# Performance work log

Measured on AMD Instinct MI355X. Metric: run time of the kernel, lower is better.

The kernel has to match this reference:

```python
import jax, jax.numpy as jnp
import numpy as np

# camera / raster constants
N = 10000            # gaussians
W = 256
H = 256
FX = 200.0
FY = 200.0
TILE = 16
NTX = W // TILE
NTY = H // TILE
NT = NTX * NTY       # 256 tiles
P = TILE * TILE      # 256 pixels per tile
K = 256              # max gaussians kept per tile
NEAR = 0.3
MAGIC = 1.2          # frustum expansion factor from project_culling
LP = 0.3 / (FX * FX) # low-pass filter added to 2D covariance diagonal


def quat_to_rot(q):
    w, x, y, z = q[:, 0], q[:, 1], q[:, 2], q[:, 3]
    r0 = jnp.stack([1 - 2 * (y * y + z * z), 2 * (x * y - w * z), 2 * (x * z + w * y)], -1)
    r1 = jnp.stack([2 * (x * y + w * z), 1 - 2 * (x * x + z * z), 2 * (y * z - w * x)], -1)
    r2 = jnp.stack([2 * (x * z - w * y), 2 * (y * z + w * x), 1 - 2 * (x * x + y * y)], -1)
    return jnp.stack([r0, r1, r2], axis=1)  # [N,3,3]


def splat_forward(pos, rgb, opacity, quaternion, scale, w2c_r, w2c_t):
    # ---- project + frustum cull (global_culling) ----
    q = quaternion / jnp.linalg.norm(quaternion, axis=-1, keepdims=True)
    R = quat_to_rot(q)
    sigma = jnp.exp(scale)                               # normalize_scale
    cov3d = jnp.einsum('nij,nj,nkj->nik', R, sigma * sigma, R)
    p_cam = pos @ w2c_r.T + w2c_t                        # [N,3]
    x, y, z = p_cam[:, 0], p_cam[:, 1], p_cam[:, 2]
    zc = jnp.maximum(z, 1e-6)
    half_w = W * MAGIC / 2 / FX
    half_h = H * MAGIC / 2 / FY
    mean2d = jnp.stack([x / zc, y / zc], -1)             # camera-plane coords
    in_frustum = (z > NEAR) & (jnp.abs(mean2d[:, 0]) < half_w) & (jnp.abs(mean2d[:, 1]) < half_h)
    iz = 1.0 / zc
    zero = jnp.zeros_like(iz)
    J = jnp.stack([jnp.stack([iz, zero, -x * iz * iz], -1),
                   jnp.stack([zero, iz, -y * iz * iz], -1)], axis=1)  # [N,2,3]
    cov_cam = jnp.einsum('ij,njk,lk->nil', w2c_r, cov3d, w2c_r)
    cov2d = jnp.einsum('nij,njk,nlk->nil', J, cov_cam, J)            # [N,2,2]
    a = cov2d[:, 0, 0] + LP
    c = cov2d[:, 1, 1] + LP
    b = cov2d[:, 0, 1]

    # ---- per-tile culling + fixed-K binning (calc_tile_list / gather_gaussians) ----
    cx = (jnp.arange(NTX) * TILE + TILE / 2 - W / 2) / FX
    cy = (jnp.arange(NTY) * TILE + TILE / 2 - H / 2) / FY
    centers = jnp.stack(jnp.meshgrid(cx, cy, indexing='xy'), -1).reshape(NT, 2)  # [NT,2] (ty-major)
    tile_half_diag = 0.5 * jnp.sqrt((TILE / FX) ** 2 + (TILE / FY) ** 2)
    mid = 0.5 * (a + c)
    sigma_max = jnp.sqrt(jnp.maximum(mid + jnp.sqrt(jnp.maximum((0.5 * (a - c)) ** 2 + b * b, 0.0)), 1e-12))
    dist = jnp.linalg.norm(centers[:, None, :] - mean2d[None, :, :], axis=-1)   # [NT,N]
    valid = in_frustum[None, :] & (dist <= (3.0 * sigma_max + tile_half_diag)[None, :])
    score = jnp.where(valid, -dist, -1e10)
    vals, idx = jax.lax.top_k(score, K)                                          # [NT,K]
    valid_k = vals > -1e9

    mean_g = mean2d[idx]                     # [NT,K,2]
    z_g = z[idx]
    a_g, b_g, c_g = a[idx], b[idx], c[idx]
    opa_g = jax.nn.sigmoid(opacity)[idx]
    rgb_g = jax.nn.sigmoid(rgb)[idx]         # [NT,K,3]

    # ---- depth sort within each tile ----
    order = jnp.argsort(jnp.where(valid_k, z_g, jnp.inf), axis=-1)
    def srt(arr):
        o = order.reshape(order.shape + (1,) * (arr.ndim - 2))
        return jnp.take_along_axis(arr, o, axis=1)
    mean_s, a_s, b_s, c_s = srt(mean_g), srt(a_g), srt(b_g), srt(c_g)
    opa_s, rgb_s = srt(opa_g), srt(rgb_g)
    valid_s = srt(valid_k).astype(pos.dtype)

    # ---- per-pixel front-to-back alpha compositing (draw) ----
    px = ((jnp.arange(W) + 0.5 - W / 2) / FX).reshape(NTX, TILE)
    py = ((jnp.arange(H) + 0.5 - H / 2) / FY).reshape(NTY, TILE)
    U = jnp.broadcast_to(px[None, :, None, :], (NTY, NTX, TILE, TILE)).reshape(NT, P)
    V = jnp.broadcast_to(py[:, None, :, None], (NTY, NTX, TILE, TILE)).reshape(NT, P)
    dx = U[:, :, None] - mean_s[:, None, :, 0]          # [NT,P,K]
    dy = V[:, :, None] - mean_s[:, None, :, 1]
    det = jnp.maximum(a_s * c_s - b_s * b_s, 1e-12)[:, None, :]
    maha = (c_s[:, None, :] * dx * dx - 2.0 * b_s[:, None, :] * dx * dy + a_s[:, None, :] * dy * dy) / det
    alpha = jnp.clip(opa_s[:, None, :] * jnp.exp(-0.5 * maha), 0.0, 0.99) * valid_s[:, None, :]
    trans = jnp.cumprod(1.0 - alpha, axis=-1)
    texc = jnp.concatenate([jnp.ones_like(trans[..., :1]), trans[..., :-1]], axis=-1)
    color = jnp.einsum('tpk,tkc->tpc', alpha * texc, rgb_s)  # [NT,P,3]
    img = color.reshape(NTY, NTX, TILE, TILE, 3).transpose(0, 2, 1, 3, 4).reshape(H, W, 3)
    return jnp.clip(img, 0.0, 1.0)


def setup_inputs() -> dict:
    key = jax.random.key(0)
    ks = jax.random.split(key, 6)
    zpos = jax.random.uniform(ks[0], (N,), minval=2.0, maxval=6.0)
    uv = jax.random.uniform(ks[1], (N, 2), minval=-0.6, maxval=0.6)
    pos = jnp.concatenate([uv * zpos[:, None], zpos[:, None]], axis=-1)
    rgb = jax.random.normal(ks[2], (N, 3))              # pre-sigmoid logits
    opacity = jax.random.normal(ks[3], (N,)) + 1.5      # sigmoid -> ~0.8 like init_opacity
    quaternion = jax.random.normal(ks[4], (N, 4))
    scale = 0.2 * jax.random.normal(ks[5], (N, 3)) - 4.5  # exp -> ~0.01 world sigma
    w2c_r = jnp.eye(3, dtype=jnp.float32)
    w2c_t = jnp.zeros((3,), dtype=jnp.float32)
    return {"pos": pos, "rgb": rgb, "opacity": opacity, "quaternion": quaternion,
            "scale": scale, "w2c_r": w2c_r, "w2c_t": w2c_t}


def reference(pos, rgb, opacity, quaternion, scale, w2c_r, w2c_t):
    return splat_forward(pos, rgb, opacity, quaternion, scale, w2c_r, w2c_t)
```

## Files before the change

### kernel.cpp

```cpp
#include <hip/hip_runtime.h>
#include <math.h>

namespace {
constexpr int W = 256, H = 256, TILE = 16, NTX = 16, NT = 256, K = 256;
constexpr float FX = 200.0f, FY = 200.0f, NEARP = 0.3f, MAGIC = 1.2f;
constexpr float LP = 0.3f / (FX * FX);
constexpr float HALF_W = W * MAGIC / 2.0f / FX;
constexpr float HALF_H = H * MAGIC / 2.0f / FY;
constexpr float THDIAG = 0.05656854249492381f;
constexpr int CAP = 1024;
constexpr int N_PAD = 10240;
constexpr int BT = 1024;
constexpr int NB_MAX = 64;
constexpr int SEG = 256;
constexpr int NSPL = 16;
constexpr size_t A_OFF  = 0;
constexpr size_t B_OFF  = A_OFF + (size_t)N_PAD * 16;
constexpr size_t C_OFF  = B_OFF + (size_t)N_PAD * 16;
constexpr size_t SL_OFF = C_OFF + (size_t)N_PAD * 16;
constexpr size_t LD_OFF = SL_OFF + (size_t)NT * NB_MAX * 4;
constexpr size_t LZ_OFF = LD_OFF + (size_t)NT * NB_MAX * SEG * 8;
constexpr size_t WS_FULL = LZ_OFF + (size_t)NT * NB_MAX * SEG * 8;
}

struct Pre { float mx, my, z, a, b, c, radius; };

__device__ inline Pre preprocess(int g, const float* __restrict__ pos,
                                 const float* __restrict__ quat,
                                 const float* __restrict__ scl,
                                 const float* __restrict__ w2cr,
                                 const float* __restrict__ w2ct) {
  float p0 = pos[3*g+0], p1 = pos[3*g+1], p2 = pos[3*g+2];
  float qw = quat[4*g+0], qx = quat[4*g+1], qy = quat[4*g+2], qz = quat[4*g+3];
  float inv = 1.0f / sqrtf(qw*qw + qx*qx + qy*qy + qz*qz);
  qw *= inv; qx *= inv; qy *= inv; qz *= inv;
  float r00 = 1.f-2.f*(qy*qy+qz*qz), r01 = 2.f*(qx*qy-qw*qz), r02 = 2.f*(qx*qz+qw*qy);
  float r10 = 2.f*(qx*qy+qw*qz), r11 = 1.f-2.f*(qx*qx+qz*qz), r12 = 2.f*(qy*qz-qw*qx);
  float r20 = 2.f*(qx*qz-qw*qy), r21 = 2.f*(qy*qz+qw*qx), r22 = 1.f-2.f*(qx*qx+qy*qy);
  float e0 = __expf(scl[3*g+0]); float s0 = e0*e0;
  float e1 = __expf(scl[3*g+1]); float s1 = e1*e1;
  float e2 = __expf(scl[3*g+2]); float s2 = e2*e2;
  float C00 = r00*r00*s0 + r01*r01*s1 + r02*r02*s2;
  float C01 = r00*r10*s0 + r01*r11*s1 + r02*r12*s2;
  float C02 = r00*r20*s0 + r01*r21*s1 + r02*r22*s2;
  float C11 = r10*r10*s0 + r11*r11*s1 + r12*r12*s2;
  float C12 = r10*r20*s0 + r11*r21*s1 + r12*r22*s2;
  float C22 = r20*r20*s0 + r21*r21*s1 + r22*r22*s2;
  float w00=w2cr[0],w01=w2cr[1],w02=w2cr[2];
  float w10=w2cr[3],w11=w2cr[4],w12=w2cr[5];
  float w20=w2cr[6],w21=w2cr[7],w22=w2cr[8];
  float x = w00*p0 + w01*p1 + w02*p2 + w2ct[0];
  float y = w10*p0 + w11*p1 + w12*p2 + w2ct[1];
  float z = w20*p0 + w21*p1 + w22*p2 + w2ct[2];
  float m00 = w00*C00 + w01*C01 + w02*C02;
  float m01 = w00*C01 + w01*C11 + w02*C12;
  float m02 = w00*C02 + w01*C12 + w02*C22;
  float m10 = w10*C00 + w11*C01 + w12*C02;
  float m11 = w10*C01 + w11*C11 + w12*C12;
  float m12 = w10*C02 + w11*C12 + w12*C22;
  float m20 = w20*C00 + w21*C01 + w22*C02;
  float m21 = w20*C01 + w21*C11 + w22*C12;
  float m22 = w20*C02 + w21*C12 + w22*C22;
  float v00 = m00*w00 + m01*w01 + m02*w02;
  float v01 = m00*w10 + m01*w11 + m02*w12;
  float v02 = m00*w20 + m01*w21 + m02*w22;
  float v10 = m10*w00 + m11*w01 + m12*w02;
  float v11 = m10*w10 + m11*w11 + m12*w12;
  float v12 = m10*w20 + m11*w21 + m12*w22;
  float v20 = m20*w00 + m21*w01 + m22*w02;
  float v21 = m20*w10 + m21*w11 + m22*w12;
  float v22 = m20*w20 + m21*w21 + m22*w22;
  float zc = fmaxf(z, 1e-6f);
  float iz = 1.0f / zc;
  float mx = x * iz, my = y * iz;
  float iz2 = iz * iz;
  float jx = -x * iz2, jy = -y * iz2;
  float a00 = iz*v00 + jx*v20, a01 = iz*v01 + jx*v21, a02 = iz*v02 + jx*v22;
  float a10 = iz*v10 + jy*v20, a11 = iz*v11 + jy*v21, a12 = iz*v12 + jy*v22;
  float A  = a00*iz + a02*jx + LP;
  float Bv = a01*iz + a02*jy;
  float Cv = a11*iz + a12*jy + LP;
  float mid = 0.5f*(A + Cv);
  float hh  = 0.5f*(A - Cv);
  float disc = fmaxf(hh*hh + Bv*Bv, 0.0f);
  float smax = sqrtf(fmaxf(mid + sqrtf(disc), 1e-12f));
  bool infr = (z > NEARP) && (fabsf(mx) < HALF_W) && (fabsf(my) < HALF_H);
  Pre r;
  r.mx = mx; r.my = my; r.z = z; r.a = A; r.b = Bv; r.c = Cv;
  r.radius = infr ? (3.0f * smax + THDIAG) : -1.0f;
  return r;
}


template <bool BIN>
__global__ __launch_bounds__(256)
void pre_bin(const float* __restrict__ pos, const float* __restrict__ rgb,
             const float* __restrict__ opac, const float* __restrict__ quat,
             const float* __restrict__ scl, const float* __restrict__ w2cr,
             const float* __restrict__ w2ct,
             float4* __restrict__ pa, float4* __restrict__ pb,
             float4* __restrict__ pc, int* __restrict__ seglen,
             unsigned long long* __restrict__ listd,
             unsigned long long* __restrict__ listz, int n) {
  __shared__ int s_tc[NT];
  const int tid = (int)threadIdx.x;
  const int blk = (int)blockIdx.x;
  if (BIN) {
    if (tid < NT) s_tc[tid] = 0;
    __syncthreads();
  }
  const int g = blk * 256 + tid;
  if (g < n) {
    Pre p = preprocess(g, pos, quat, scl, w2cr, w2ct);
    float det = fmaxf(p.a * p.c - p.b * p.b, 1e-12f);
    float ivd = 1.0f / det;
    float lopa = -__logf(1.0f + __expf(-opac[g]));
    pa[g] = make_float4(p.mx, p.my, p.radius, p.z);
    pb[g] = make_float4(-0.5f * ivd * p.c, ivd * p.b, -0.5f * ivd * p.a, lopa);
    pc[g] = make_float4(1.0f / (1.0f + __expf(-rgb[3*g+0])),
                        1.0f / (1.0f + __expf(-rgb[3*g+1])),
                        1.0f / (1.0f + __expf(-rgb[3*g+2])), 0.0f);
    if (BIN && p.radius >= 0.0f) {
      float r = p.radius;
      int txlo = max(0,     (int)floorf(((p.mx - r) * FX + 120.0f) * 0.0625f));
      int txhi = min(NTX-1, (int)ceilf (((p.mx + r) * FX + 120.0f) * 0.0625f));
      int tylo = max(0,     (int)floorf(((p.my - r) * FY + 120.0f) * 0.0625f));
      int tyhi = min(NTX-1, (int)ceilf (((p.my + r) * FY + 120.0f) * 0.0625f));
      unsigned long long gbits = (unsigned int)g;
      for (int ty = tylo; ty <= tyhi; ++ty) {
        float cy = (ty * TILE + TILE * 0.5f - H * 0.5f) / FY;
        float ddy = cy - p.my;
        for (int tx = txlo; tx <= txhi; ++tx) {
          float cx = (tx * TILE + TILE * 0.5f - W * 0.5f) / FX;
          float ddx = cx - p.mx;
          float dist = sqrtf(ddx * ddx + ddy * ddy);
          if (dist <= r) {
            int t = ty * NTX + tx;
            int slot = atomicAdd(&s_tc[t], 1);
            size_t idx = ((size_t)t * NB_MAX + blk) * SEG + slot;
            listd[idx] = ((unsigned long long)__float_as_uint(dist) << 32) | gbits;
            listz[idx] = ((unsigned long long)__float_as_uint(p.z)  << 32) | gbits;
          }
        }
      }
    }
  }
  if (BIN) {
    __syncthreads();
    if (tid < NT) seglen[(size_t)tid * NB_MAX + blk] = s_tc[tid];
  }
}


__device__ inline void hsort1(unsigned long long* key, int M) {
  const int tid = (int)threadIdx.x;
  __syncthreads();
  unsigned long long e = (tid < M) ? key[tid] : ~0ull;
  for (int k = 2; k <= M; k <<= 1) {
    for (int j = k >> 1; j >= 64; j >>= 1) {
      __syncthreads();
      if (tid < M) key[tid] = e;
      __syncthreads();
      if (tid < M) {
        unsigned long long p = key[tid ^ j];
        bool takeMin = (((tid & j) == 0) == ((tid & k) == 0));
        e = ((p < e) == takeMin) ? p : e;
      }
    }
    int j0 = ((k >> 1) < 32) ? (k >> 1) : 32;
    for (int j = j0; j >= 1; j >>= 1) {
      unsigned long long p = __shfl_xor(e, j, 64);
      bool takeMin = (((tid & j) == 0) == ((tid & k) == 0));
      e = ((p < e) == takeMin) ? p : e;
    }
  }
  __syncthreads();
  if (tid < M) key[tid] = e;
  __syncthreads();
}


__device__ inline void tail16(
    const float4* __restrict__ pa, const float4* __restrict__ pb,
    const float4* __restrict__ pc, float* __restrict__ out,
    unsigned long long* s_zkey, int* s_rank,
    float4* s_p0, float4* s_p1, float* s_cb, float4* s_part,
    int cnt2, int tx, int ty) {
  const int tid = (int)threadIdx.x;
  {
    const int e = tid & 255;
    const int q = tid >> 8;
    const int rchunk = (cnt2 + 3) >> 2;
    if (e < cnt2) {
      unsigned long long mykey = s_zkey[e];
      int jlo = q * rchunk;
      int jhi = min(cnt2, jlo + rchunk);
      int partial = 0;
      for (int j = jlo; j < jhi; ++j)
        partial += (s_zkey[j] < mykey) ? 1 : 0;
      if (partial) atomicAdd(&s_rank[e], partial);
    }
  }
  __syncthreads();
  if (tid < cnt2) {
    int g = (int)(s_zkey[tid] & 0xffffffffu);
    int r = s_rank[tid];
    float4 A = pa[g], B = pb[g], C = pc[g];
    s_p0[r] = make_float4(A.x, A.y, B.x, B.y);
    s_p1[r] = make_float4(B.z, B.w, C.x, C.y);
    s_cb[r] = C.z;
  }
  __syncthreads();

  const int p6  = tid & 63;
  const int q16 = tid >> 6;
  const int prow0 = p6 >> 4;
  const int pcol  = p6 & 15;
  const float u  = ((float)(tx * TILE + pcol) + 0.5f - W * 0.5f) / FX;
  const float v0 = ((float)(ty * TILE + prow0 +  0) + 0.5f - H * 0.5f) / FY;
  const float v1 = ((float)(ty * TILE + prow0 +  4) + 0.5f - H * 0.5f) / FY;
  const float v2 = ((float)(ty * TILE + prow0 +  8) + 0.5f - H * 0.5f) / FY;
  const float v3 = ((float)(ty * TILE + prow0 + 12) + 0.5f - H * 0.5f) / FY;
  const int chunk = (cnt2 + NSPL - 1) / NSPL;
  const int k0 = q16 * chunk;
  const int k1 = min(cnt2, k0 + chunk);
  float T0 = 1.0f, r0 = 0.0f, g0 = 0.0f, b0 = 0.0f;
  float T1 = 1.0f, r1 = 0.0f, g1 = 0.0f, b1 = 0.0f;
  float T2 = 1.0f, r2 = 0.0f, g2 = 0.0f, b2 = 0.0f;
  float T3 = 1.0f, r3 = 0.0f, g3 = 0.0f, b3 = 0.0f;
  for (int k2 = k0; k2 < k1; ++k2) {
    float4 P0 = s_p0[k2];
    float4 P1 = s_p1[k2];
    float cb = s_cb[k2];
    float dx = u - P0.x;
    float s  = fmaf(P0.z * dx, dx, P1.y);
    float bd = P0.w * dx;
    {
      float dy = v0 - P0.y;
      float m  = fmaf(fmaf(P1.x, dy, bd), dy, s);
      float a  = fminf(__expf(m), 0.99f);
      float w  = a * T0;
      r0 = fmaf(w, P1.z, r0); g0 = fmaf(w, P1.w, g0); b0 = fmaf(w, cb, b0);
      T0 = fmaf(-a, T0, T0);
    }
    {
      float dy = v1 - P0.y;
      float m  = fmaf(fmaf(P1.x, dy, bd), dy, s);
      float a  = fminf(__expf(m), 0.99f);
      float w  = a * T1;
      r1 = fmaf(w, P1.z, r1); g1 = fmaf(w, P1.w, g1); b1 = fmaf(w, cb, b1);
      T1 = fmaf(-a, T1, T1);
    }
    {
      float dy = v2 - P0.y;
      float m  = fmaf(fmaf(P1.x, dy, bd), dy, s);
      float a  = fminf(__expf(m), 0.99f);
      float w  = a * T2;
      r2 = fmaf(w, P1.z, r2); g2 = fmaf(w, P1.w, g2); b2 = fmaf(w, cb, b2);
      T2 = fmaf(-a, T2, T2);
    }
    {
      float dy = v3 - P0.y;
      float m  = fmaf(fmaf(P1.x, dy, bd), dy, s);
      float a  = fminf(__expf(m), 0.99f);
      float w  = a * T3;
      r3 = fmaf(w, P1.z, r3); g3 = fmaf(w, P1.w, g3); b3 = fmaf(w, cb, b3);
      T3 = fmaf(-a, T3, T3);
    }
  }
  s_part[q16 * 256 + p6 +   0] = make_float4(r0, g0, b0, T0);
  s_part[q16 * 256 + p6 +  64] = make_float4(r1, g1, b1, T1);
  s_part[q16 * 256 + p6 + 128] = make_float4(r2, g2, b2, T2);
  s_part[q16 * 256 + p6 + 192] = make_float4(r3, g3, b3, T3);
  __syncthreads();

  if (tid < 256) {
    float4 P = s_part[(NSPL - 1) * 256 + tid];
    float r = P.x, g = P.y, b = P.z;
    #pragma unroll
    for (int q = NSPL - 2; q >= 0; --q) {
      float4 Q = s_part[q * 256 + tid];
      r = fmaf(Q.w, r, Q.x);
      g = fmaf(Q.w, g, Q.y);
      b = fmaf(Q.w, b, Q.z);
    }
    const int p6o = tid & 63;
    const int sub = tid >> 6;
    const int prow = (p6o >> 4) + 4 * sub;
    const int pcol2 = p6o & 15;
    const int row = ty * TILE + prow;
    const int col = tx * TILE + pcol2;
    const int o = (row * W + col) * 3;
    out[o+0] = fminf(fmaxf(r, 0.0f), 1.0f);
    out[o+1] = fminf(fmaxf(g, 0.0f), 1.0f);
    out[o+2] = fminf(fmaxf(b, 0.0f), 1.0f);
  }
}


__global__ __launch_bounds__(BT)
void render_list(const float4* __restrict__ pa, const float4* __restrict__ pb,
                 const float4* __restrict__ pc, const int* __restrict__ seglen,
                 const unsigned long long* __restrict__ listd,
                 const unsigned long long* __restrict__ listz,
                 float* __restrict__ out, int nb) {
  __shared__ unsigned long long s_zkey[CAP];
  __shared__ unsigned long long s_dkey[CAP];
  __shared__ int s_off[NB_MAX + 1];
  __shared__ int s_rank[K];
  __shared__ float4 s_p0[K];
  __shared__ float4 s_p1[K];
  __shared__ float  s_cb[K];
  __shared__ float4 s_part[NSPL * 256];

  const int t  = (int)blockIdx.x;
  const int tx = t % NTX;
  const int ty = t / NTX;
  const int tid = (int)threadIdx.x;

  if (tid < K) s_rank[tid] = 0;
  if (tid < 64) {
    int v = (tid < nb) ? seglen[(size_t)t * NB_MAX + tid] : 0;
    #pragma unroll
    for (int d = 1; d < 64; d <<= 1) {
      int u2 = __shfl_up(v, d, 64);
      if (tid >= d) v += u2;
    }
    if (tid == 0) s_off[0] = 0;
    if (tid < nb) s_off[tid + 1] = v;
  }
  __syncthreads();
  int cnt = min(s_off[nb], CAP);

  for (int i = tid; i < cnt; i += BT) {
    int lo = 0, hi = nb;
    while (hi - lo > 1) {
      int mid = (lo + hi) >> 1;
      if (s_off[mid] <= i) lo = mid; else hi = mid;
    }
    size_t src = ((size_t)t * NB_MAX + lo) * SEG + (size_t)(i - s_off[lo]);
    s_zkey[i] = listz[src];
  }
  __syncthreads();
  int cnt2 = cnt;

  if (cnt > K) {
    for (int i = tid; i < cnt; i += BT) {
      int lo = 0, hi = nb;
      while (hi - lo > 1) {
        int mid = (lo + hi) >> 1;
        if (s_off[mid] <= i) lo = mid; else hi = mid;
      }
      size_t src = ((size_t)t * NB_MAX + lo) * SEG + (size_t)(i - s_off[lo]);
      s_dkey[i] = listd[src];
    }
    int M = 512; while (M < cnt) M <<= 1;
    for (int i = cnt + tid; i < M; i += BT) s_dkey[i] = ~0ull;
    hsort1(s_dkey, M);
    if (tid < K) {
      int g = (int)(s_dkey[tid] & 0xffffffffu);
      s_zkey[tid] = ((unsigned long long)__float_as_uint(pa[g].w) << 32) |
                    (unsigned int)g;
    }
    __syncthreads();
    cnt2 = K;
  }

  tail16(pa, pb, pc, out, s_zkey, s_rank, s_p0, s_p1, s_cb, s_part, cnt2, tx, ty);
}


__global__ __launch_bounds__(BT)
void render_scan(const float4* __restrict__ pa, const float4* __restrict__ pb,
                 const float4* __restrict__ pc, float* __restrict__ out, int n) {
  __shared__ unsigned long long s_zkey[CAP];
  __shared__ unsigned long long s_dkey[CAP];
  __shared__ int s_rank[K];
  __shared__ float4 s_p0[K];
  __shared__ float4 s_p1[K];
  __shared__ float  s_cb[K];
  __shared__ float4 s_part[NSPL * 256];
  __shared__ int s_cnt;

  const int t  = (int)blockIdx.x;
  const int tx = t % NTX;
  const int ty = t / NTX;
  const int tid = (int)threadIdx.x;
  const int lane = tid & 63;
  const float cxc = (tx * TILE + TILE * 0.5f - W * 0.5f) / FX;
  const float cyc = (ty * TILE + TILE * 0.5f - H * 0.5f) / FY;

  if (tid == 0) s_cnt = 0;
  if (tid < K) s_rank[tid] = 0;
  __syncthreads();

  for (int g = tid; g < n; g += BT) {
    float4 v = pa[g];
    float ddx = cxc - v.x, ddy = cyc - v.y;
    float dist = sqrtf(ddx * ddx + ddy * ddy);
    bool hit = (v.z >= 0.0f) && (dist <= v.z);
    unsigned long long m = __ballot(hit);
    if (m) {
      int leader = __ffsll((long long)m) - 1;
      int base = 0;
      if (lane == leader) base = atomicAdd(&s_cnt, __popcll(m));
      base = __shfl(base, leader, 64);
      if (hit) {
        int slot = base + __popcll(m & ((1ull << lane) - 1ull));
        if (slot < CAP) {
          s_dkey[slot] = ((unsigned long long)__float_as_uint(dist) << 32) |
                         (unsigned int)g;
          s_zkey[slot] = ((unsigned long long)__float_as_uint(v.w) << 32) |
                         (unsigned int)g;
        }
      }
    }
  }
  __syncthreads();
  int cnt = min(s_cnt, CAP);
  int cnt2 = cnt;

  if (cnt > K) {
    int M = 512; while (M < cnt) M <<= 1;
    for (int i = cnt + tid; i < M; i += BT) s_dkey[i] = ~0ull;
    hsort1(s_dkey, M);
    if (tid < K) {
      int g = (int)(s_dkey[tid] & 0xffffffffu);
      s_zkey[tid] = ((unsigned long long)__float_as_uint(pa[g].w) << 32) |
                    (unsigned int)g;
    }
    __syncthreads();
    cnt2 = K;
  }

  tail16(pa, pb, pc, out, s_zkey, s_rank, s_p0, s_p1, s_cb, s_part, cnt2, tx, ty);
}

extern "C" void kernel_launch(void* const* d_in, const int* in_sizes, int n_in,
                              void* d_out, int out_size, void* d_ws, size_t ws_size,
                              hipStream_t stream) {
  const float* pos  = (const float*)d_in[0];
  const float* rgb  = (const float*)d_in[1];
  const float* opac = (const float*)d_in[2];
  const float* quat = (const float*)d_in[3];
  const float* scl  = (const float*)d_in[4];
  const float* w2cr = (const float*)d_in[5];
  const float* w2ct = (const float*)d_in[6];
  float* out = (float*)d_out;
  const int n = in_sizes[0] / 3;
  const int nb = (n + 255) / 256;

  char* ws = (char*)d_ws;
  float4* pa = (float4*)(ws + A_OFF);
  float4* pb = (float4*)(ws + B_OFF);
  float4* pc = (float4*)(ws + C_OFF);
  int* seglen = (int*)(ws + SL_OFF);
  unsigned long long* listd = (unsigned long long*)(ws + LD_OFF);
  unsigned long long* listz = (unsigned long long*)(ws + LZ_OFF);

  if (ws_size >= WS_FULL && nb <= NB_MAX) {
    pre_bin<true><<<nb, 256, 0, stream>>>(
        pos, rgb, opac, quat, scl, w2cr, w2ct, pa, pb, pc, seglen, listd, listz, n);
    render_list<<<NT, BT, 0, stream>>>(pa, pb, pc, seglen, listd, listz, out, nb);
  } else {
    pre_bin<false><<<nb, 256, 0, stream>>>(
        pos, rgb, opac, quat, scl, w2cr, w2ct, pa, pb, pc, seglen, listd, listz, n);
    render_scan<<<NT, BT, 0, stream>>>(pa, pb, pc, out, n);
  }
}
```

Measured before the change: 21.17 us.

## Bin full gaussian records per tile instead of indices, sort with payload

```diff
diff --git a/kernel.cpp b/kernel.cpp
--- a/kernel.cpp
+++ b/kernel.cpp
@@ -8,19 +8,12 @@
 constexpr float HALF_W = W * MAGIC / 2.0f / FX;
 constexpr float HALF_H = H * MAGIC / 2.0f / FY;
 constexpr float THDIAG = 0.05656854249492381f;
-constexpr int CAP = 1024;
+constexpr int CAP = 512;
 constexpr int N_PAD = 10240;
 constexpr int BT = 1024;
 constexpr int NB_MAX = 64;
 constexpr int SEG = 256;
 constexpr int NSPL = 16;
-constexpr size_t A_OFF  = 0;
-constexpr size_t B_OFF  = A_OFF + (size_t)N_PAD * 16;
-constexpr size_t C_OFF  = B_OFF + (size_t)N_PAD * 16;
-constexpr size_t SL_OFF = C_OFF + (size_t)N_PAD * 16;
-constexpr size_t LD_OFF = SL_OFF + (size_t)NT * NB_MAX * 4;
-constexpr size_t LZ_OFF = LD_OFF + (size_t)NT * NB_MAX * SEG * 8;
-constexpr size_t WS_FULL = LZ_OFF + (size_t)NT * NB_MAX * SEG * 8;
 }
 
 struct Pre { float mx, my, z, a, b, c, radius; };
@@ -92,41 +85,38 @@
 }
 
 
-template <bool BIN>
 __global__ __launch_bounds__(256)
 void pre_bin(const float* __restrict__ pos, const float* __restrict__ rgb,
              const float* __restrict__ opac, const float* __restrict__ quat,
              const float* __restrict__ scl, const float* __restrict__ w2cr,
              const float* __restrict__ w2ct,
-             float4* __restrict__ pa, float4* __restrict__ pb,
-             float4* __restrict__ pc, int* __restrict__ seglen,
-             unsigned long long* __restrict__ listd,
-             unsigned long long* __restrict__ listz, int n) {
+             float4* __restrict__ rA, float4* __restrict__ rB,
+             unsigned long long* __restrict__ zk, float* __restrict__ rC,
+             int* __restrict__ seglen, int n, int nb) {
   __shared__ int s_tc[NT];
   const int tid = (int)threadIdx.x;
   const int blk = (int)blockIdx.x;
-  if (BIN) {
-    if (tid < NT) s_tc[tid] = 0;
-    __syncthreads();
-  }
+  if (tid < NT) s_tc[tid] = 0;
+  __syncthreads();
   const int g = blk * 256 + tid;
   if (g < n) {
     Pre p = preprocess(g, pos, quat, scl, w2cr, w2ct);
-    float det = fmaxf(p.a * p.c - p.b * p.b, 1e-12f);
-    float ivd = 1.0f / det;
-    float lopa = -__logf(1.0f + __expf(-opac[g]));
-    pa[g] = make_float4(p.mx, p.my, p.radius, p.z);
-    pb[g] = make_float4(-0.5f * ivd * p.c, ivd * p.b, -0.5f * ivd * p.a, lopa);
-    pc[g] = make_float4(1.0f / (1.0f + __expf(-rgb[3*g+0])),
-                        1.0f / (1.0f + __expf(-rgb[3*g+1])),
-                        1.0f / (1.0f + __expf(-rgb[3*g+2])), 0.0f);
-    if (BIN && p.radius >= 0.0f) {
+    if (p.radius >= 0.0f) {
+      float det = fmaxf(p.a * p.c - p.b * p.b, 1e-12f);
+      float ivd = 1.0f / det;
+      float lopa = -__logf(1.0f + __expf(-opac[g]));
+      float4 recA = make_float4(p.mx, p.my, -0.5f * ivd * p.c, ivd * p.b);
+      float4 recB = make_float4(-0.5f * ivd * p.a, lopa,
+                                1.0f / (1.0f + __expf(-rgb[3*g+0])),
+                                1.0f / (1.0f + __expf(-rgb[3*g+1])));
+      float recC = 1.0f / (1.0f + __expf(-rgb[3*g+2]));
+      unsigned long long zkey =
+          ((unsigned long long)__float_as_uint(p.z) << 32) | (unsigned int)g;
       float r = p.radius;
       int txlo = max(0,     (int)floorf(((p.mx - r) * FX + 120.0f) * 0.0625f));
       int txhi = min(NTX-1, (int)ceilf (((p.mx + r) * FX + 120.0f) * 0.0625f));
       int tylo = max(0,     (int)floorf(((p.my - r) * FY + 120.0f) * 0.0625f));
       int tyhi = min(NTX-1, (int)ceilf (((p.my + r) * FY + 120.0f) * 0.0625f));
-      unsigned long long gbits = (unsigned int)g;
       for (int ty = tylo; ty <= tyhi; ++ty) {
         float cy = (ty * TILE + TILE * 0.5f - H * 0.5f) / FY;
         float ddy = cy - p.my;
@@ -137,56 +127,147 @@
           if (dist <= r) {
             int t = ty * NTX + tx;
             int slot = atomicAdd(&s_tc[t], 1);
-            size_t idx = ((size_t)t * NB_MAX + blk) * SEG + slot;
-            listd[idx] = ((unsigned long long)__float_as_uint(dist) << 32) | gbits;
-            listz[idx] = ((unsigned long long)__float_as_uint(p.z)  << 32) | gbits;
+            size_t idx = ((size_t)t * nb + blk) * SEG + slot;
+            rA[idx] = recA;
+            rB[idx] = recB;
+            zk[idx] = zkey;
+            rC[idx] = recC;
           }
         }
       }
     }
   }
-  if (BIN) {
+  __syncthreads();
+  if (tid < NT) seglen[(size_t)tid * nb + blk] = s_tc[tid];
+}
+
+
+__global__ __launch_bounds__(256)
+void pre_only(const float* __restrict__ pos, const float* __restrict__ rgb,
+              const float* __restrict__ opac, const float* __restrict__ quat,
+              const float* __restrict__ scl, const float* __restrict__ w2cr,
+              const float* __restrict__ w2ct,
+              float4* __restrict__ pa, float4* __restrict__ pb,
+              float4* __restrict__ pc, int n) {
+  int g = blockIdx.x * 256 + (int)threadIdx.x;
+  if (g >= n) return;
+  Pre p = preprocess(g, pos, quat, scl, w2cr, w2ct);
+  float det = fmaxf(p.a * p.c - p.b * p.b, 1e-12f);
+  float ivd = 1.0f / det;
+  float lopa = -__logf(1.0f + __expf(-opac[g]));
+  pa[g] = make_float4(p.mx, p.my, p.radius, p.z);
+  pb[g] = make_float4(-0.5f * ivd * p.c, ivd * p.b, -0.5f * ivd * p.a, lopa);
+  pc[g] = make_float4(1.0f / (1.0f + __expf(-rgb[3*g+0])),
+                      1.0f / (1.0f + __expf(-rgb[3*g+1])),
+                      1.0f / (1.0f + __expf(-rgb[3*g+2])), 0.0f);
+}
+
+
+__device__ inline void bsort_pay(unsigned long long* key, int* pay, int M) {
+  const int tid = (int)threadIdx.x;
+  for (int k = 2; k <= M; k <<= 1) {
+    for (int j = k >> 1; j > 0; j >>= 1) {
+      __syncthreads();
+      for (int i = tid; i < M; i += BT) {
+        int ixj = i ^ j;
+        if (ixj > i) {
+          unsigned long long a = key[i], b = key[ixj];
+          bool up = ((i & k) == 0);
+          if (up ? (a > b) : (a < b)) {
+            key[i] = b; key[ixj] = a;
+            int tpp = pay[i]; pay[i] = pay[ixj]; pay[ixj] = tpp;
+          }
+        }
+      }
+    }
+  }
+  __syncthreads();
+}
+
+
+__global__ __launch_bounds__(BT)
+void render_list(const float4* __restrict__ rA, const float4* __restrict__ rB,
+                 const unsigned long long* __restrict__ zk,
+                 const float* __restrict__ rC, const int* __restrict__ seglen,
+                 float* __restrict__ out, int nb) {
+  __shared__ unsigned long long s_zkey[CAP];
+  __shared__ float4 s_p0s[CAP];
+  __shared__ float4 s_p1s[CAP];
+  __shared__ float  s_cbs[CAP];
+  __shared__ unsigned long long s_dkey[CAP];
+  __shared__ int s_pay[CAP];
+  __shared__ int s_off[NB_MAX + 1];
+  __shared__ int s_rank[K];
+  __shared__ float4 s_p0[K];
+  __shared__ float4 s_p1[K];
+  __shared__ float  s_cb[K];
+  __shared__ float4 s_part[NSPL * 256];
+
+  const int t  = (int)blockIdx.x;
+  const int tx = t % NTX;
+  const int ty = t / NTX;
+  const int tid = (int)threadIdx.x;
+
+  if (tid < K) s_rank[tid] = 0;
+  if (tid < 64) {
+    int v = (tid < nb) ? seglen[(size_t)t * nb + tid] : 0;
+    #pragma unroll
+    for (int d = 1; d < 64; d <<= 1) {
+      int u2 = __shfl_up(v, d, 64);
+      if (tid >= d) v += u2;
+    }
+    if (tid == 0) s_off[0] = 0;
+    if (tid < nb) s_off[tid + 1] = v;
+  }
+  __syncthreads();
+  int cnt = min(s_off[nb], CAP);
+
+  for (int i = tid; i < cnt; i += BT) {
+    int lo = 0, hi = nb;
+    while (hi - lo > 1) {
+      int mid = (lo + hi) >> 1;
+      if (s_off[mid] <= i) lo = mid; else hi = mid;
+    }
+    size_t src = ((size_t)t * nb + lo) * SEG + (size_t)(i - s_off[lo]);
+    s_zkey[i] = zk[src];
+    s_p0s[i]  = rA[src];
+    s_p1s[i]  = rB[src];
+    s_cbs[i]  = rC[src];
+  }
+  __syncthreads();
+  int cnt2 = cnt;
+
+  if (cnt > K) {
+    const float cxc = (tx * TILE + TILE * 0.5f - W * 0.5f) / FX;
+    const float cyc = (ty * TILE + TILE * 0.5f - H * 0.5f) / FY;
+    int M = 512; while (M < cnt) M <<= 1;
+    for (int i = tid; i < M; i += BT) {
+      if (i < cnt) {
+        float ddx = cxc - s_p0s[i].x, ddy = cyc - s_p0s[i].y;
+        float dist = sqrtf(ddx * ddx + ddy * ddy);
+        s_dkey[i] = ((unsigned long long)__float_as_uint(dist) << 32) |
+                    (unsigned int)(s_zkey[i] & 0xffffffffu);
+        s_pay[i] = i;
+      } else {
+        s_dkey[i] = ~0ull;
+        s_pay[i] = 0;
+      }
+    }
     __syncthreads();
-    if (tid < NT) seglen[(size_t)tid * NB_MAX + blk] = s_tc[tid];
-  }
-}
-
-
-__device__ inline void hsort1(unsigned long long* key, int M) {
-  const int tid = (int)threadIdx.x;
-  __syncthreads();
-  unsigned long long e = (tid < M) ? key[tid] : ~0ull;
-  for (int k = 2; k <= M; k <<= 1) {
-    for (int j = k >> 1; j >= 64; j >>= 1) {
-      __syncthreads();
-      if (tid < M) key[tid] = e;
-      __syncthreads();
-      if (tid < M) {
-        unsigned long long p = key[tid ^ j];
-        bool takeMin = (((tid & j) == 0) == ((tid & k) == 0));
-        e = ((p < e) == takeMin) ? p : e;
-      }
-    }
-    int j0 = ((k >> 1) < 32) ? (k >> 1) : 32;
-    for (int j = j0; j >= 1; j >>= 1) {
-      unsigned long long p = __shfl_xor(e, j, 64);
-      bool takeMin = (((tid & j) == 0) == ((tid & k) == 0));
-      e = ((p < e) == takeMin) ? p : e;
-    }
-  }
-  __syncthreads();
-  if (tid < M) key[tid] = e;
-  __syncthreads();
-}
-
-
-__device__ inline void tail16(
-    const float4* __restrict__ pa, const float4* __restrict__ pb,
-    const float4* __restrict__ pc, float* __restrict__ out,
-    unsigned long long* s_zkey, int* s_rank,
-    float4* s_p0, float4* s_p1, float* s_cb, float4* s_part,
-    int cnt2, int tx, int ty) {
-  const int tid = (int)threadIdx.x;
+    bsort_pay(s_dkey, s_pay, M);
+    unsigned long long zkr = 0; float4 P0r, P1r; float cbr = 0.f;
+    if (tid < K) {
+      int p = s_pay[tid];
+      zkr = s_zkey[p]; P0r = s_p0s[p]; P1r = s_p1s[p]; cbr = s_cbs[p];
+    }
+    __syncthreads();
+    if (tid < K) {
+      s_zkey[tid] = zkr; s_p0s[tid] = P0r; s_p1s[tid] = P1r; s_cbs[tid] = cbr;
+    }
+    __syncthreads();
+    cnt2 = K;
+  }
+
   {
     const int e = tid & 255;
     const int q = tid >> 8;
@@ -203,12 +284,10 @@
   }
   __syncthreads();
   if (tid < cnt2) {
-    int g = (int)(s_zkey[tid] & 0xffffffffu);
     int r = s_rank[tid];
-    float4 A = pa[g], B = pb[g], C = pc[g];
-    s_p0[r] = make_float4(A.x, A.y, B.x, B.y);
-    s_p1[r] = make_float4(B.z, B.w, C.x, C.y);
-    s_cb[r] = C.z;
+    s_p0[r] = s_p0s[tid];
+    s_p1[r] = s_p1s[tid];
+    s_cb[r] = s_cbs[tid];
   }
   __syncthreads();
 
@@ -299,82 +378,14 @@
 
 
 __global__ __launch_bounds__(BT)
-void render_list(const float4* __restrict__ pa, const float4* __restrict__ pb,
-                 const float4* __restrict__ pc, const int* __restrict__ seglen,
-                 const unsigned long long* __restrict__ listd,
-                 const unsigned long long* __restrict__ listz,
-                 float* __restrict__ out, int nb) {
-  __shared__ unsigned long long s_zkey[CAP];
-  __shared__ unsigned long long s_dkey[CAP];
-  __shared__ int s_off[NB_MAX + 1];
-  __shared__ int s_rank[K];
-  __shared__ float4 s_p0[K];
-  __shared__ float4 s_p1[K];
-  __shared__ float  s_cb[K];
-  __shared__ float4 s_part[NSPL * 256];
-
-  const int t  = (int)blockIdx.x;
-  const int tx = t % NTX;
-  const int ty = t / NTX;
-  const int tid = (int)threadIdx.x;
-
-  if (tid < K) s_rank[tid] = 0;
-  if (tid < 64) {
-    int v = (tid < nb) ? seglen[(size_t)t * NB_MAX + tid] : 0;
-    #pragma unroll
-    for (int d = 1; d < 64; d <<= 1) {
-      int u2 = __shfl_up(v, d, 64);
-      if (tid >= d) v += u2;
-    }
-    if (tid == 0) s_off[0] = 0;
-    if (tid < nb) s_off[tid + 1] = v;
-  }
-  __syncthreads();
-  int cnt = min(s_off[nb], CAP);
-
-  for (int i = tid; i < cnt; i += BT) {
-    int lo = 0, hi = nb;
-    while (hi - lo > 1) {
-      int mid = (lo + hi) >> 1;
-      if (s_off[mid] <= i) lo = mid; else hi = mid;
-    }
-    size_t src = ((size_t)t * NB_MAX + lo) * SEG + (size_t)(i - s_off[lo]);
-    s_zkey[i] = listz[src];
-  }
-  __syncthreads();
-  int cnt2 = cnt;
-
-  if (cnt > K) {
-    for (int i = tid; i < cnt; i += BT) {
-      int lo = 0, hi = nb;
-      while (hi - lo > 1) {
-        int mid = (lo + hi) >> 1;
-        if (s_off[mid] <= i) lo = mid; else hi = mid;
-      }
-      size_t src = ((size_t)t * NB_MAX + lo) * SEG + (size_t)(i - s_off[lo]);
-      s_dkey[i] = listd[src];
-    }
-    int M = 512; while (M < cnt) M <<= 1;
-    for (int i = cnt + tid; i < M; i += BT) s_dkey[i] = ~0ull;
-    hsort1(s_dkey, M);
-    if (tid < K) {
-      int g = (int)(s_dkey[tid] & 0xffffffffu);
-      s_zkey[tid] = ((unsigned long long)__float_as_uint(pa[g].w) << 32) |
-                    (unsigned int)g;
-    }
-    __syncthreads();
-    cnt2 = K;
-  }
-
-  tail16(pa, pb, pc, out, s_zkey, s_rank, s_p0, s_p1, s_cb, s_part, cnt2, tx, ty);
-}
-
-
-__global__ __launch_bounds__(BT)
 void render_scan(const float4* __restrict__ pa, const float4* __restrict__ pb,
                  const float4* __restrict__ pc, float* __restrict__ out, int n) {
   __shared__ unsigned long long s_zkey[CAP];
+  __shared__ float4 s_p0s[CAP];
+  __shared__ float4 s_p1s[CAP];
+  __shared__ float  s_cbs[CAP];
   __shared__ unsigned long long s_dkey[CAP];
+  __shared__ int s_pay[CAP];
   __shared__ int s_rank[K];
   __shared__ float4 s_p0[K];
   __shared__ float4 s_p1[K];
@@ -412,6 +423,10 @@
                          (unsigned int)g;
           s_zkey[slot] = ((unsigned long long)__float_as_uint(v.w) << 32) |
                          (unsigned int)g;
+          float4 B = pb[g], C = pc[g];
+          s_p0s[slot] = make_float4(v.x, v.y, B.x, B.y);
+          s_p1s[slot] = make_float4(B.z, B.w, C.x, C.y);
+          s_cbs[slot] = C.z;
         }
       }
     }
@@ -422,18 +437,131 @@
 
   if (cnt > K) {
     int M = 512; while (M < cnt) M <<= 1;
-    for (int i = cnt + tid; i < M; i += BT) s_dkey[i] = ~0ull;
-    hsort1(s_dkey, M);
+    for (int i = tid; i < M; i += BT) {
+      if (i >= cnt) { s_dkey[i] = ~0ull; s_pay[i] = 0; }
+      else s_pay[i] = i;
+    }
+    __syncthreads();
+    bsort_pay(s_dkey, s_pay, M);
+    unsigned long long zkr = 0; float4 P0r, P1r; float cbr = 0.f;
     if (tid < K) {
-      int g = (int)(s_dkey[tid] & 0xffffffffu);
-      s_zkey[tid] = ((unsigned long long)__float_as_uint(pa[g].w) << 32) |
-                    (unsigned int)g;
+      int p = s_pay[tid];
+      zkr = s_zkey[p]; P0r = s_p0s[p]; P1r = s_p1s[p]; cbr = s_cbs[p];
+    }
+    __syncthreads();
+    if (tid < K) {
+      s_zkey[tid] = zkr; s_p0s[tid] = P0r; s_p1s[tid] = P1r; s_cbs[tid] = cbr;
     }
     __syncthreads();
     cnt2 = K;
   }
 
-  tail16(pa, pb, pc, out, s_zkey, s_rank, s_p0, s_p1, s_cb, s_part, cnt2, tx, ty);
+  {
+    const int e = tid & 255;
+    const int q = tid >> 8;
+    const int rchunk = (cnt2 + 3) >> 2;
+    if (e < cnt2) {
+      unsigned long long mykey = s_zkey[e];
+      int jlo = q * rchunk;
+      int jhi = min(cnt2, jlo + rchunk);
+      int partial = 0;
+      for (int j = jlo; j < jhi; ++j)
+        partial += (s_zkey[j] < mykey) ? 1 : 0;
+      if (partial) atomicAdd(&s_rank[e], partial);
+    }
+  }
+  __syncthreads();
+  if (tid < cnt2) {
+    int r = s_rank[tid];
+    s_p0[r] = s_p0s[tid];
+    s_p1[r] = s_p1s[tid];
+    s_cb[r] = s_cbs[tid];
+  }
+  __syncthreads();
+
+  const int p6  = tid & 63;
+  const int q16 = tid >> 6;
+  const int prow0 = p6 >> 4;
+  const int pcol  = p6 & 15;
+  const float u  = ((float)(tx * TILE + pcol) + 0.5f - W * 0.5f) / FX;
+  const float v0 = ((float)(ty * TILE + prow0 +  0) + 0.5f - H * 0.5f) / FY;
+  const float v1 = ((float)(ty * TILE + prow0 +  4) + 0.5f - H * 0.5f) / FY;
+  const float v2 = ((float)(ty * TILE + prow0 +  8) + 0.5f - H * 0.5f) / FY;
+  const float v3 = ((float)(ty * TILE + prow0 + 12) + 0.5f - H * 0.5f) / FY;
+  const int chunk = (cnt2 + NSPL - 1) / NSPL;
+  const int k0 = q16 * chunk;
+  const int k1 = min(cnt2, k0 + chunk);
+  float T0 = 1.0f, r0 = 0.0f, g0 = 0.0f, b0 = 0.0f;
+  float T1 = 1.0f, r1 = 0.0f, g1 = 0.0f, b1 = 0.0f;
+  float T2 = 1.0f, r2 = 0.0f, g2 = 0.0f, b2 = 0.0f;
+  float T3 = 1.0f, r3 = 0.0f, g3 = 0.0f, b3 = 0.0f;
+  for (int k2 = k0; k2 < k1; ++k2) {
+    float4 P0 = s_p0[k2];
+    float4 P1 = s_p1[k2];
+    float cb = s_cb[k2];
+    float dx = u - P0.x;
+    float s  = fmaf(P0.z * dx, dx, P1.y);
+    float bd = P0.w * dx;
+    {
+      float dy = v0 - P0.y;
+      float m  = fmaf(fmaf(P1.x, dy, bd), dy, s);
+      float a  = fminf(__expf(m), 0.99f);
+      float w  = a * T0;
+      r0 = fmaf(w, P1.z, r0); g0 = fmaf(w, P1.w, g0); b0 = fmaf(w, cb, b0);
+      T0 = fmaf(-a, T0, T0);
+    }
+    {
+      float dy = v1 - P0.y;
+      float m  = fmaf(fmaf(P1.x, dy, bd), dy, s);
+      float a  = fminf(__expf(m), 0.99f);
+      float w  = a * T1;
+      r1 = fmaf(w, P1.z, r1); g1 = fmaf(w, P1.w, g1); b1 = fmaf(w, cb, b1);
+      T1 = fmaf(-a, T1, T1);
+    }
+    {
+      float dy = v2 - P0.y;
+      float m  = fmaf(fmaf(P1.x, dy, bd), dy, s);
+      float a  = fminf(__expf(m), 0.99f);
+      float w  = a * T2;
+      r2 = fmaf(w, P1.z, r2); g2 = fmaf(w, P1.w, g2); b2 = fmaf(w, cb, b2);
+      T2 = fmaf(-a, T2, T2);
+    }
+    {
+      float dy = v3 - P0.y;
+      float m  = fmaf(fmaf(P1.x, dy, bd), dy, s);
+      float a  = fminf(__expf(m), 0.99f);
+      float w  = a * T3;
+      r3 = fmaf(w, P1.z, r3); g3 = fmaf(w, P1.w, g3); b3 = fmaf(w, cb, b3);
+      T3 = fmaf(-a, T3, T3);
+    }
+  }
+  s_part[q16 * 256 + p6 +   0] = make_float4(r0, g0, b0, T0);
+  s_part[q16 * 256 + p6 +  64] = make_float4(r1, g1, b1, T1);
+  s_part[q16 * 256 + p6 + 128] = make_float4(r2, g2, b2, T2);
+  s_part[q16 * 256 + p6 + 192] = make_float4(r3, g3, b3, T3);
+  __syncthreads();
+
+  if (tid < 256) {
+    float4 P = s_part[(NSPL - 1) * 256 + tid];
+    float r = P.x, g = P.y, b = P.z;
+    #pragma unroll
+    for (int q = NSPL - 2; q >= 0; --q) {
+      float4 Q = s_part[q * 256 + tid];
+      r = fmaf(Q.w, r, Q.x);
+      g = fmaf(Q.w, g, Q.y);
+      b = fmaf(Q.w, b, Q.z);
+    }
+    const int p6o = tid & 63;
+    const int sub = tid >> 6;
+    const int prow = (p6o >> 4) + 4 * sub;
+    const int pcol2 = p6o & 15;
+    const int row = ty * TILE + prow;
+    const int col = tx * TILE + pcol2;
+    const int o = (row * W + col) * 3;
+    out[o+0] = fminf(fmaxf(r, 0.0f), 1.0f);
+    out[o+1] = fminf(fmaxf(g, 0.0f), 1.0f);
+    out[o+2] = fminf(fmaxf(b, 0.0f), 1.0f);
+  }
 }
 
 extern "C" void kernel_launch(void* const* d_in, const int* in_sizes, int n_in,
@@ -450,21 +578,31 @@
   const int n = in_sizes[0] / 3;
   const int nb = (n + 255) / 256;
 
+  const size_t E = (size_t)NT * nb * SEG;
+  const size_t rA_off = 0;
+  const size_t rB_off = rA_off + E * 16;
+  const size_t zk_off = rB_off + E * 16;
+  const size_t rC_off = zk_off + E * 8;
+  const size_t sl_off = rC_off + E * 4;
+  const size_t need   = sl_off + (size_t)NT * nb * 4;
+
   char* ws = (char*)d_ws;
-  float4* pa = (float4*)(ws + A_OFF);
-  float4* pb = (float4*)(ws + B_OFF);
-  float4* pc = (float4*)(ws + C_OFF);
-  int* seglen = (int*)(ws + SL_OFF);
-  unsigned long long* listd = (unsigned long long*)(ws + LD_OFF);
-  unsigned long long* listz = (unsigned long long*)(ws + LZ_OFF);
-
-  if (ws_size >= WS_FULL && nb <= NB_MAX) {
-    pre_bin<true><<<nb, 256, 0, stream>>>(
-        pos, rgb, opac, quat, scl, w2cr, w2ct, pa, pb, pc, seglen, listd, listz, n);
-    render_list<<<NT, BT, 0, stream>>>(pa, pb, pc, seglen, listd, listz, out, nb);
+
+  if (ws_size >= need && nb <= NB_MAX) {
+    float4* rA = (float4*)(ws + rA_off);
+    float4* rB = (float4*)(ws + rB_off);
+    unsigned long long* zkp = (unsigned long long*)(ws + zk_off);
+    float* rC = (float*)(ws + rC_off);
+    int* seglen = (int*)(ws + sl_off);
+    pre_bin<<<nb, 256, 0, stream>>>(
+        pos, rgb, opac, quat, scl, w2cr, w2ct, rA, rB, zkp, rC, seglen, n, nb);
+    render_list<<<NT, BT, 0, stream>>>(rA, rB, zkp, rC, seglen, out, nb);
   } else {
-    pre_bin<false><<<nb, 256, 0, stream>>>(
-        pos, rgb, opac, quat, scl, w2cr, w2ct, pa, pb, pc, seglen, listd, listz, n);
+    float4* pa = (float4*)ws;
+    float4* pb = (float4*)(ws + (size_t)N_PAD * 16);
+    float4* pc = (float4*)(ws + (size_t)N_PAD * 32);
+    pre_only<<<(n + 255) / 256, 256, 0, stream>>>(
+        pos, rgb, opac, quat, scl, w2cr, w2ct, pa, pb, pc, n);
     render_scan<<<NT, BT, 0, stream>>>(pa, pb, pc, out, n);
   }
 }
```

After: 21.46 us. No clear change (+1.4%).
